# Performance work log

Hardware: AMD Instinct MI355X
Metric: run time of the kernel (lower is better)

Reference implementation:

```python
import jax, jax.numpy as jnp
import numpy as np

E = 20000
EDGE_DIM = 16
CH_IN = 32
CH_OUT = 32
T_IN = 1
T_OUT = 1
D_IN = 2 * T_IN + 1      # 3
D_OUT = 2 * T_OUT + 1    # 3
NUM_FREQ = 2 * min(T_IN, T_OUT) + 1  # 3
EPS = 1e-5


def setup_inputs() -> dict:
    key = jax.random.key(0)
    ks = jax.random.split(key, 6)
    return {
        "f": jax.random.normal(ks[0], (E, EDGE_DIM + 1), dtype=jnp.float32),
        "basis": jax.random.normal(ks[1], (E, 1, D_OUT, 1, D_IN, NUM_FREQ), dtype=jnp.float32),
        "w1": jax.random.normal(ks[2], (32, EDGE_DIM + 1), dtype=jnp.float32) * (2.0 / (EDGE_DIM + 1)) ** 0.5,
        "b1": jnp.zeros((32,), jnp.float32),
        "g1": jnp.ones((32,), jnp.float32),
        "be1": jnp.zeros((32,), jnp.float32),
        "w2": jax.random.normal(ks[3], (32, 32), dtype=jnp.float32) * (2.0 / 32) ** 0.5,
        "b2": jnp.zeros((32,), jnp.float32),
        "g2": jnp.ones((32,), jnp.float32),
        "be2": jnp.zeros((32,), jnp.float32),
        "w3": jax.random.normal(ks[4], (NUM_FREQ * CH_IN * CH_OUT, 32), dtype=jnp.float32) * (2.0 / 32) ** 0.5,
        "b3": jnp.zeros((NUM_FREQ * CH_IN * CH_OUT,), jnp.float32),
    }


def _layernorm(x, g, b):
    mu = jnp.mean(x, axis=-1, keepdims=True)
    var = jnp.mean(jnp.square(x - mu), axis=-1, keepdims=True)
    return (x - mu) * jax.lax.rsqrt(var + EPS) * g + b


def reference(f, basis, w1, b1, g1, be1, w2, b2, g2, be2, w3, b3):
    # Radial MLP: Linear -> LN -> ReLU -> Linear -> LN -> ReLU -> Linear
    h = jax.nn.relu(_layernorm(f @ w1.T + b1, g1, be1))
    h = jax.nn.relu(_layernorm(h @ w2.T + b2, g2, be2))
    r = h @ w3.T + b3                                 # [E, ch_out*ch_in*num_freq]
    R = r.reshape(E, CH_OUT, CH_IN, NUM_FREQ)
    B = basis.reshape(E, D_OUT, D_IN, NUM_FREQ)       # squeeze broadcast dims
    # contraction over num_freq without the (E,co,do,ci,di,nf) blowup
    kernel = jnp.einsum('ecdf,epqf->ecpdq', R, B)     # [E, ch_out, d_out, ch_in, d_in]
    return kernel.reshape(E, D_OUT * CH_OUT, CH_IN * D_IN)
```

## Files before the change

kernel.cpp:

```cpp
#include <hip/hip_runtime.h>

#define EB 4
#define NT 384
#define W3S 36

struct F3 { float x, y, z; };

__global__ __launch_bounds__(NT) void singleconv_fused(
    const float* __restrict__ f,
    const float* __restrict__ basis,
    const float* __restrict__ w1,
    const float* __restrict__ b1,
    const float* __restrict__ g1,
    const float* __restrict__ be1,
    const float* __restrict__ w2,
    const float* __restrict__ b2,
    const float* __restrict__ g2,
    const float* __restrict__ be2,
    const float* __restrict__ w3,
    const float* __restrict__ b3,
    float* __restrict__ out)
{
    __shared__ float sf[EB][17];
    __shared__ float sbas[EB][27];
    __shared__ float sh1[EB][32];
    __shared__ alignas(16) float sh2[EB][32];
    __shared__ alignas(16) float sw3[2][96 * W3S];
    __shared__ float sr[EB * 96];

    const int t  = threadIdx.x;
    const int e0 = blockIdx.x * EB;

    const int re   = t / 96;
    const int rcol = t - re * 96;
    const int wrow = t >> 2;
    const int wk   = (t & 3) * 8;

    float4 pa, pb;
    {
        const float4* ws = (const float4*)(w3);
        pa = ws[t * 2];
        pb = ws[t * 2 + 1];
    }
    float bnx = b3[rcol];

    if (t < EB * 17) { int e = t / 17, i = t - e * 17; sf[e][i] = f[(e0 + e) * 17 + i]; }
    if (t >= 128 && t < 128 + EB * 27) {
        int q = t - 128, e = q / 27, i = q - e * 27;
        sbas[e][i] = basis[(e0 + e) * 27 + i];
    }
    __syncthreads();

    if (t < EB * 32) {
        int e = t >> 5, j = t & 31;
        float acc = b1[j];
        #pragma unroll
        for (int k = 0; k < 17; k++) acc += sf[e][k] * w1[j * 17 + k];
        float s = acc;
        #pragma unroll
        for (int m = 16; m >= 1; m >>= 1) s += __shfl_xor(s, m);
        float mu = s * (1.f / 32.f);
        float d  = acc - mu;
        float v  = d * d;
        #pragma unroll
        for (int m = 16; m >= 1; m >>= 1) v += __shfl_xor(v, m);
        float rs = rsqrtf(v * (1.f / 32.f) + 1e-5f);
        sh1[e][j] = fmaxf(d * rs * g1[j] + be1[j], 0.f);
    }
    __syncthreads();

    if (t < EB * 32) {
        int e = t >> 5, j = t & 31;
        float acc = b2[j];
        #pragma unroll
        for (int k = 0; k < 32; k++) acc += sh1[e][k] * w2[j * 32 + k];
        float s = acc;
        #pragma unroll
        for (int m = 16; m >= 1; m >>= 1) s += __shfl_xor(s, m);
        float mu = s * (1.f / 32.f);
        float d  = acc - mu;
        float v  = d * d;
        #pragma unroll
        for (int m = 16; m >= 1; m >>= 1) v += __shfl_xor(v, m);
        float rs = rsqrtf(v * (1.f / 32.f) + 1e-5f);
        sh2[e][j] = fmaxf(d * rs * g2[j] + be2[j], 0.f);
    }
    __syncthreads();

    float4 hv[8];
    {
        const float4* hp = (const float4*)(&sh2[re][0]);
        #pragma unroll
        for (int k = 0; k < 8; k++) hv[k] = hp[k];
    }

    const int dord = rcol >> 5;
    const int ci   = t & 31;
    float br[3][3];
    {
        const float* bp = &sbas[re][dord * 9];
        #pragma unroll
        for (int q = 0; q < 9; q++) (&br[0][0])[q] = bp[q];
    }
    const float* rp = &sr[re * 96 + ci * 3];
    float* op = out + (size_t)(e0 + re) * 9216 + dord * 96 + ci * 3;

    int buf = 0;
    for (int co = 0; co < 32; ++co) {
        float* wd = &sw3[buf][wrow * W3S + wk];
        *(float4*)(wd)     = pa;
        *(float4*)(wd + 4) = pb;
        float bcur = bnx;

        int cn = (co + 1) & 31;
        const float4* ws = (const float4*)(w3 + cn * 3072);
        pa  = ws[t * 2];
        pb  = ws[t * 2 + 1];
        bnx = b3[cn * 96 + rcol];

        __syncthreads();

        float acc = bcur;
        const float* wp = &sw3[buf][rcol * W3S];
        #pragma unroll
        for (int k = 0; k < 8; k++) {
            float4 w = *(const float4*)(wp + k * 4);
            acc += w.x * hv[k].x + w.y * hv[k].y + w.z * hv[k].z + w.w * hv[k].w;
        }
        sr[t] = acc;
        __syncthreads();

        float r0 = rp[0], r1 = rp[1], r2 = rp[2];
        F3 o;
        o.x = r0 * br[0][0] + r1 * br[0][1] + r2 * br[0][2];
        o.y = r0 * br[1][0] + r1 * br[1][1] + r2 * br[1][2];
        o.z = r0 * br[2][0] + r1 * br[2][1] + r2 * br[2][2];
        *(F3*)(op + co * 288) = o;

        buf ^= 1;
    }
}

extern "C" void kernel_launch(void* const* d_in, const int* in_sizes, int n_in,
                              void* d_out, int out_size, void* d_ws, size_t ws_size,
                              hipStream_t stream) {
    const float* f     = (const float*)d_in[0];
    const float* basis = (const float*)d_in[1];
    const float* w1    = (const float*)d_in[2];
    const float* b1    = (const float*)d_in[3];
    const float* g1    = (const float*)d_in[4];
    const float* be1   = (const float*)d_in[5];
    const float* w2    = (const float*)d_in[6];
    const float* b2    = (const float*)d_in[7];
    const float* g2    = (const float*)d_in[8];
    const float* be2   = (const float*)d_in[9];
    const float* w3    = (const float*)d_in[10];
    const float* b3    = (const float*)d_in[11];
    float* out = (float*)d_out;

    dim3 grid(20000 / EB), block(NT);
    hipLaunchKernelGGL(singleconv_fused, grid, block, 0, stream,
                       f, basis, w1, b1, g1, be1, w2, b2, g2, be2, w3, b3, out);
}
```

Measured before the change: 858.4 us.

## Process 16 edges per block so each staged w3 tile serves more edges

```diff
diff --git a/kernel.cpp b/kernel.cpp
--- a/kernel.cpp
+++ b/kernel.cpp
@@ -1,6 +1,6 @@
 #include <hip/hip_runtime.h>
 
-#define EB 4
+#define EB 16
 #define NT 384
 #define W3S 36
 
@@ -25,14 +25,14 @@
     __shared__ float sbas[EB][27];
     __shared__ float sh1[EB][32];
     __shared__ alignas(16) float sh2[EB][32];
-    __shared__ alignas(16) float sw3[2][96 * W3S];
+    __shared__ alignas(16) float sw3[96 * W3S];
     __shared__ float sr[EB * 96];
 
     const int t  = threadIdx.x;
     const int e0 = blockIdx.x * EB;
 
-    const int re   = t / 96;
-    const int rcol = t - re * 96;
+    const int rcol = t % 96;
+    const int eg   = t / 96;
     const int wrow = t >> 2;
     const int wk   = (t & 3) * 8;
 
@@ -45,14 +45,14 @@
     float bnx = b3[rcol];
 
     if (t < EB * 17) { int e = t / 17, i = t - e * 17; sf[e][i] = f[(e0 + e) * 17 + i]; }
-    if (t >= 128 && t < 128 + EB * 27) {
-        int q = t - 128, e = q / 27, i = q - e * 27;
+    for (int q = t; q < EB * 27; q += NT) {
+        int e = q / 27, i = q - e * 27;
         sbas[e][i] = basis[(e0 + e) * 27 + i];
     }
     __syncthreads();
 
-    if (t < EB * 32) {
-        int e = t >> 5, j = t & 31;
+    for (int slot = t; slot < EB * 32; slot += NT) {
+        int e = slot >> 5, j = slot & 31;
         float acc = b1[j];
         #pragma unroll
         for (int k = 0; k < 17; k++) acc += sf[e][k] * w1[j * 17 + k];
@@ -69,8 +69,8 @@
     }
     __syncthreads();
 
-    if (t < EB * 32) {
-        int e = t >> 5, j = t & 31;
+    for (int slot = t; slot < EB * 32; slot += NT) {
+        int e = slot >> 5, j = slot & 31;
         float acc = b2[j];
         #pragma unroll
         for (int k = 0; k < 32; k++) acc += sh1[e][k] * w2[j * 32 + k];
@@ -87,27 +87,26 @@
     }
     __syncthreads();
 
-    float4 hv[8];
-    {
-        const float4* hp = (const float4*)(&sh2[re][0]);
+    const int dord = rcol >> 5;
+    const int ci   = rcol & 31;
+    float br[4][9];
+    const float* rpp[4];
+    float* opp[4];
+    #pragma unroll
+    for (int s = 0; s < 4; s++) {
+        int e = eg + 4 * s;
+        const float* bp = &sbas[e][dord * 9];
         #pragma unroll
-        for (int k = 0; k < 8; k++) hv[k] = hp[k];
+        for (int q = 0; q < 9; q++) br[s][q] = bp[q];
+        rpp[s] = &sr[e * 96 + ci * 3];
+        opp[s] = out + (size_t)(e0 + e) * 9216 + dord * 96 + ci * 3;
     }
 
-    const int dord = rcol >> 5;
-    const int ci   = t & 31;
-    float br[3][3];
-    {
-        const float* bp = &sbas[re][dord * 9];
-        #pragma unroll
-        for (int q = 0; q < 9; q++) (&br[0][0])[q] = bp[q];
-    }
-    const float* rp = &sr[re * 96 + ci * 3];
-    float* op = out + (size_t)(e0 + re) * 9216 + dord * 96 + ci * 3;
+    const int eb  = eg * 4;
+    const int srb = eb * 96 + rcol;
 
-    int buf = 0;
     for (int co = 0; co < 32; ++co) {
-        float* wd = &sw3[buf][wrow * W3S + wk];
+        float* wd = &sw3[wrow * W3S + wk];
         *(float4*)(wd)     = pa;
         *(float4*)(wd + 4) = pb;
         float bcur = bnx;
@@ -120,24 +119,37 @@
 
         __syncthreads();
 
-        float acc = bcur;
-        const float* wp = &sw3[buf][rcol * W3S];
+        float a0 = bcur, a1 = bcur, a2 = bcur, a3 = bcur;
+        const float* wp = &sw3[rcol * W3S];
         #pragma unroll
         for (int k = 0; k < 8; k++) {
-            float4 w = *(const float4*)(wp + k * 4);
-            acc += w.x * hv[k].x + w.y * hv[k].y + w.z * hv[k].z + w.w * hv[k].w;
+            float4 w  = *(const float4*)(wp + k * 4);
+            float4 h0 = *(const float4*)(&sh2[eb + 0][k * 4]);
+            float4 h1 = *(const float4*)(&sh2[eb + 1][k * 4]);
+            float4 h2v= *(const float4*)(&sh2[eb + 2][k * 4]);
+            float4 h3 = *(const float4*)(&sh2[eb + 3][k * 4]);
+            a0 += w.x * h0.x  + w.y * h0.y  + w.z * h0.z  + w.w * h0.w;
+            a1 += w.x * h1.x  + w.y * h1.y  + w.z * h1.z  + w.w * h1.w;
+            a2 += w.x * h2v.x + w.y * h2v.y + w.z * h2v.z + w.w * h2v.w;
+            a3 += w.x * h3.x  + w.y * h3.y  + w.z * h3.z  + w.w * h3.w;
         }
-        sr[t] = acc;
+        sr[srb]       = a0;
+        sr[srb + 96]  = a1;
+        sr[srb + 192] = a2;
+        sr[srb + 288] = a3;
+
         __syncthreads();
 
-        float r0 = rp[0], r1 = rp[1], r2 = rp[2];
-        F3 o;
-        o.x = r0 * br[0][0] + r1 * br[0][1] + r2 * br[0][2];
-        o.y = r0 * br[1][0] + r1 * br[1][1] + r2 * br[1][2];
-        o.z = r0 * br[2][0] + r1 * br[2][1] + r2 * br[2][2];
-        *(F3*)(op + co * 288) = o;
-
-        buf ^= 1;
+        const int orow = co * 288;
+        #pragma unroll
+        for (int s = 0; s < 4; s++) {
+            float r0 = rpp[s][0], r1 = rpp[s][1], r2 = rpp[s][2];
+            F3 o;
+            o.x = r0 * br[s][0] + r1 * br[s][1] + r2 * br[s][2];
+            o.y = r0 * br[s][3] + r1 * br[s][4] + r2 * br[s][5];
+            o.z = r0 * br[s][6] + r1 * br[s][7] + r2 * br[s][8];
+            *(F3*)(opp[s] + orow) = o;
+        }
     }
 }
 
```

After: 844.2 us. No clear change (-1.7%).
